# Kernel tuning notes

Measured on AMD Instinct MI355X. Metric: run time of the kernel, lower is better.

The kernel has to match this reference:

```python
import jax, jax.numpy as jnp
import numpy as np

M = 8192
K = 32

def setup_inputs() -> dict:
    key = jax.random.key(0)
    kw, ky = jax.random.split(key)
    W = jax.random.uniform(kw, (M, M), dtype=jnp.float32)  # nonnegative affinity
    Y = jax.random.normal(ky, (M, K), dtype=jnp.float32)
    return {"W": W, "Y": Y}

def reference(W, Y):
    # Random-walk Laplacian Rayleigh quotient: trace(Y^T (I - D^{-1} W) Y) / m,
    # with D = diag(row sums of W). Exploits diagonal D: D^{-1} W Y == (W @ Y) / d[:, None].
    m = Y.shape[0]
    d = jnp.sum(W, axis=1)                      # [m] row sums (diag of D)
    WY = W @ Y                                   # [m, k] thin matmul
    LY = Y - WY / d[:, None]                     # (I - D^{-1} W) Y without forming L
    loss = jnp.sum(Y * LY) / m                   # trace(Y^T L Y) / m
    return loss
```

## Files before the change

kernel.cpp:

```cpp
#include <hip/hip_runtime.h>

#define MDIM 8192
#define KD 32
#define SROW 260
#define TILES_PB 4
#define NBLOCKS 1024
#define NRED 32

typedef __attribute__((ext_vector_type(8))) short short8;
typedef __attribute__((ext_vector_type(4))) float f32x4;

__device__ __forceinline__ short f2bf(float f) {
    unsigned int u = __builtin_bit_cast(unsigned int, f);
    u = (u + 0x7FFFu + ((u >> 16) & 1u)) >> 16;
    return (short)(unsigned short)u;
}

__global__ __launch_bounds__(256)
void spectral_mfma(const float* __restrict__ W, const float* __restrict__ Y,
                   float* __restrict__ ws_s, float* __restrict__ ws_d) {
    __shared__ float YT[KD * SROW];

    const int tid  = threadIdx.x;
    const int wave = tid >> 6;
    const int lane = tid & 63;
    const int g    = lane >> 4;
    const int n    = lane & 15;

    const int rg = blockIdx.x >> 3;
    const int js = blockIdx.x & 7;
    const int rowBaseW = rg * 64 + wave * 16;
    const int rowW = rowBaseW + n;
    const float* Wrow = W + (size_t)rowW * MDIM;
    const int jbase0 = js * 1024;

    f32x4 acc1 = {0.f, 0.f, 0.f, 0.f};
    f32x4 acc2 = {0.f, 0.f, 0.f, 0.f};
    float dpart = 0.f;

    for (int tile = 0; tile < TILES_PB; ++tile) {
        const int jt = jbase0 + tile * 256;

        __syncthreads();

        float4 yr[8];
        {
            const float4* yp = (const float4*)(Y + (size_t)(jt + tid) * KD);
#pragma unroll
            for (int q = 0; q < 8; ++q) yr[q] = yp[q];
        }
        float4 wv[8][2];
#pragma unroll
        for (int jc = 0; jc < 8; ++jc) {
            const float* p = Wrow + jt + jc * 32 + g * 8;
            wv[jc][0] = *(const float4*)p;
            wv[jc][1] = *(const float4*)(p + 4);
        }
#pragma unroll
        for (int q = 0; q < 8; ++q) {
            YT[(4 * q + 0) * SROW + tid] = yr[q].x;
            YT[(4 * q + 1) * SROW + tid] = yr[q].y;
            YT[(4 * q + 2) * SROW + tid] = yr[q].z;
            YT[(4 * q + 3) * SROW + tid] = yr[q].w;
        }
        __syncthreads();

#pragma unroll
        for (int jc = 0; jc < 8; ++jc) {
            dpart += ((wv[jc][0].x + wv[jc][0].y) + (wv[jc][0].z + wv[jc][0].w))
                   + ((wv[jc][1].x + wv[jc][1].y) + (wv[jc][1].z + wv[jc][1].w));
            short8 a;
            a[0] = f2bf(wv[jc][0].x); a[1] = f2bf(wv[jc][0].y);
            a[2] = f2bf(wv[jc][0].z); a[3] = f2bf(wv[jc][0].w);
            a[4] = f2bf(wv[jc][1].x); a[5] = f2bf(wv[jc][1].y);
            a[6] = f2bf(wv[jc][1].z); a[7] = f2bf(wv[jc][1].w);

            const int jo = jc * 32 + g * 8;
            const float* b1p = &YT[n * SROW + jo];
            const float* b2p = &YT[(n + 16) * SROW + jo];
            float4 b1a = *(const float4*)b1p, b1b = *(const float4*)(b1p + 4);
            float4 b2a = *(const float4*)b2p, b2b = *(const float4*)(b2p + 4);
            short8 b1, b2;
            b1[0] = f2bf(b1a.x); b1[1] = f2bf(b1a.y); b1[2] = f2bf(b1a.z); b1[3] = f2bf(b1a.w);
            b1[4] = f2bf(b1b.x); b1[5] = f2bf(b1b.y); b1[6] = f2bf(b1b.z); b1[7] = f2bf(b1b.w);
            b2[0] = f2bf(b2a.x); b2[1] = f2bf(b2a.y); b2[2] = f2bf(b2a.z); b2[3] = f2bf(b2a.w);
            b2[4] = f2bf(b2b.x); b2[5] = f2bf(b2b.y); b2[6] = f2bf(b2b.z); b2[7] = f2bf(b2b.w);

            acc1 = __builtin_amdgcn_mfma_f32_16x16x32_bf16(a, b1, acc1, 0, 0, 0);
            acc2 = __builtin_amdgcn_mfma_f32_16x16x32_bf16(a, b2, acc2, 0, 0, 0);
        }
    }

#pragma unroll
    for (int r = 0; r < 4; ++r) {
        const int m = g * 4 + r;
        const int grow = rowBaseW + m;
        float ps = acc1[r] * Y[(size_t)grow * KD + n]
                 + acc2[r] * Y[(size_t)grow * KD + 16 + n];
        ps += __shfl_xor(ps, 1);
        ps += __shfl_xor(ps, 2);
        ps += __shfl_xor(ps, 4);
        ps += __shfl_xor(ps, 8);
        if (n == 0) atomicAdd(&ws_s[grow], ps);
    }
    float dv = dpart;
    dv += __shfl_xor(dv, 16);
    dv += __shfl_xor(dv, 32);
    if (g == 0) atomicAdd(&ws_d[rowBaseW + n], dv);
}

__global__ void zero_ws_kernel(float* __restrict__ ws_s, float* __restrict__ ws_d,
                               float* __restrict__ out) {
    const int i = blockIdx.x * 256 + threadIdx.x;
    ws_s[i] = 0.f;
    ws_d[i] = 0.f;
    if (i == 0) out[0] = 0.f;
}

__global__ void finalize_kernel(const float* __restrict__ Y,
                                const float* __restrict__ ws_s,
                                const float* __restrict__ ws_d,
                                float* __restrict__ out) {
    __shared__ float red[256];
    const int tid = threadIdx.x;
    const int i = blockIdx.x * 256 + tid;
    const float4* yp = (const float4*)(Y + (size_t)i * KD);
    float yy = 0.f;
#pragma unroll
    for (int q = 0; q < 8; ++q) {
        float4 y = yp[q];
        yy += y.x * y.x + y.y * y.y + y.z * y.z + y.w * y.w;
    }
    red[tid] = yy - ws_s[i] / ws_d[i];
    __syncthreads();
#pragma unroll
    for (int s = 128; s > 0; s >>= 1) {
        if (tid < s) red[tid] += red[tid + s];
        __syncthreads();
    }
    if (tid == 0) atomicAdd(out, red[0] * (1.0f / (float)MDIM));
}

extern "C" void kernel_launch(void* const* d_in, const int* in_sizes, int n_in,
                              void* d_out, int out_size, void* d_ws, size_t ws_size,
                              hipStream_t stream) {
    const float* W = (const float*)d_in[0];
    const float* Y = (const float*)d_in[1];
    float* out  = (float*)d_out;
    float* ws_s = (float*)d_ws;
    float* ws_d = ws_s + MDIM;

    zero_ws_kernel<<<NRED, 256, 0, stream>>>(ws_s, ws_d, out);
    spectral_mfma<<<NBLOCKS, 256, 0, stream>>>(W, Y, ws_s, ws_d);
    finalize_kernel<<<NRED, 256, 0, stream>>>(Y, ws_s, ws_d, out);
}
```

Measured before the change: 384.3 us.

## Pre-transpose Y to bf16 in global memory and compute row sums via MFMA

A prep kernel now converts Y into a transposed bf16 array in the workspace and zeroes the accumulators, replacing the separate zero kernel. The main kernel reads its B operands straight from global memory, so the shared-memory staging and both __syncthreads per tile go away. W is packed to bf16 with a truncating byte-permute instead of round-to-nearest-even, and the row sums d now come from a third MFMA against a ones vector instead of fp32 adds. The j range is split 16 ways for more blocks. In exchange, d is computed from bf16-truncated W, which costs accuracy, and B loads now hit global or cache memory instead of LDS.

```diff
diff --git a/kernel.cpp b/kernel.cpp
--- a/kernel.cpp
+++ b/kernel.cpp
@@ -2,119 +2,105 @@
 
 #define MDIM 8192
 #define KD 32
-#define SROW 260
-#define TILES_PB 4
-#define NBLOCKS 1024
+#define JSPLIT 16
+#define JWIN (MDIM / JSPLIT)
+#define NBLOCKS (128 * JSPLIT)
 #define NRED 32
 
 typedef __attribute__((ext_vector_type(8))) short short8;
 typedef __attribute__((ext_vector_type(4))) float f32x4;
 
-__device__ __forceinline__ short f2bf(float f) {
+union S8U { short8 s; uint4 u; };
+
+__device__ __forceinline__ unsigned short f2bf_rne(float f) {
     unsigned int u = __builtin_bit_cast(unsigned int, f);
     u = (u + 0x7FFFu + ((u >> 16) & 1u)) >> 16;
-    return (short)(unsigned short)u;
+    return (unsigned short)u;
+}
+
+__device__ __forceinline__ unsigned pk(float lo, float hi) {
+    return __builtin_amdgcn_perm(__builtin_bit_cast(unsigned, hi),
+                                 __builtin_bit_cast(unsigned, lo), 0x07060302u);
+}
+
+__global__ void prep_kernel(const float* __restrict__ Y, unsigned short* __restrict__ YT,
+                            float* __restrict__ ws_s, float* __restrict__ ws_d,
+                            float* __restrict__ out) {
+    const int j = blockIdx.x * 256 + threadIdx.x;
+    ws_s[j] = 0.f;
+    ws_d[j] = 0.f;
+    if (j == 0) out[0] = 0.f;
+    const float4* yp = (const float4*)(Y + (size_t)j * KD);
+#pragma unroll
+    for (int q = 0; q < 8; ++q) {
+        float4 v = yp[q];
+        YT[(size_t)(4 * q + 0) * MDIM + j] = f2bf_rne(v.x);
+        YT[(size_t)(4 * q + 1) * MDIM + j] = f2bf_rne(v.y);
+        YT[(size_t)(4 * q + 2) * MDIM + j] = f2bf_rne(v.z);
+        YT[(size_t)(4 * q + 3) * MDIM + j] = f2bf_rne(v.w);
+    }
 }
 
 __global__ __launch_bounds__(256)
-void spectral_mfma(const float* __restrict__ W, const float* __restrict__ Y,
+void spectral_mfma(const float* __restrict__ W, const unsigned short* __restrict__ YTb,
+                   const float* __restrict__ Y,
                    float* __restrict__ ws_s, float* __restrict__ ws_d) {
-    __shared__ float YT[KD * SROW];
-
     const int tid  = threadIdx.x;
     const int wave = tid >> 6;
     const int lane = tid & 63;
     const int g    = lane >> 4;
     const int n    = lane & 15;
 
-    const int rg = blockIdx.x >> 3;
-    const int js = blockIdx.x & 7;
-    const int rowBaseW = rg * 64 + wave * 16;
-    const int rowW = rowBaseW + n;
-    const float* Wrow = W + (size_t)rowW * MDIM;
-    const int jbase0 = js * 1024;
+    const int rg = blockIdx.x >> 4;
+    const int js = blockIdx.x & (JSPLIT - 1);
+    const int rowBase = rg * 64 + wave * 16;
+    const float* Wrow = W + (size_t)(rowBase + n) * MDIM;
+    const int j0 = js * JWIN;
 
     f32x4 acc1 = {0.f, 0.f, 0.f, 0.f};
     f32x4 acc2 = {0.f, 0.f, 0.f, 0.f};
-    float dpart = 0.f;
+    f32x4 acc3 = {0.f, 0.f, 0.f, 0.f};
 
-    for (int tile = 0; tile < TILES_PB; ++tile) {
-        const int jt = jbase0 + tile * 256;
+    S8U ones;
+    ones.u = make_uint4(0x3F803F80u, 0x3F803F80u, 0x3F803F80u, 0x3F803F80u);
 
-        __syncthreads();
+    const float* wp0 = Wrow + j0 + g * 8;
+    const unsigned short* bp0 = YTb + (size_t)n * MDIM + j0 + g * 8;
 
-        float4 yr[8];
-        {
-            const float4* yp = (const float4*)(Y + (size_t)(jt + tid) * KD);
-#pragma unroll
-            for (int q = 0; q < 8; ++q) yr[q] = yp[q];
-        }
-        float4 wv[8][2];
-#pragma unroll
-        for (int jc = 0; jc < 8; ++jc) {
-            const float* p = Wrow + jt + jc * 32 + g * 8;
-            wv[jc][0] = *(const float4*)p;
-            wv[jc][1] = *(const float4*)(p + 4);
-        }
-#pragma unroll
-        for (int q = 0; q < 8; ++q) {
-            YT[(4 * q + 0) * SROW + tid] = yr[q].x;
-            YT[(4 * q + 1) * SROW + tid] = yr[q].y;
-            YT[(4 * q + 2) * SROW + tid] = yr[q].z;
-            YT[(4 * q + 3) * SROW + tid] = yr[q].w;
-        }
-        __syncthreads();
+#pragma unroll 4
+    for (int it = 0; it < JWIN / 32; ++it) {
+        const float* wp = wp0 + it * 32;
+        float4 w0 = *(const float4*)wp;
+        float4 w1 = *(const float4*)(wp + 4);
+        const unsigned short* bp = bp0 + it * 32;
+        short8 b1 = *(const short8*)bp;
+        short8 b2 = *(const short8*)(bp + (size_t)16 * MDIM);
 
-#pragma unroll
-        for (int jc = 0; jc < 8; ++jc) {
-            dpart += ((wv[jc][0].x + wv[jc][0].y) + (wv[jc][0].z + wv[jc][0].w))
-                   + ((wv[jc][1].x + wv[jc][1].y) + (wv[jc][1].z + wv[jc][1].w));
-            short8 a;
-            a[0] = f2bf(wv[jc][0].x); a[1] = f2bf(wv[jc][0].y);
-            a[2] = f2bf(wv[jc][0].z); a[3] = f2bf(wv[jc][0].w);
-            a[4] = f2bf(wv[jc][1].x); a[5] = f2bf(wv[jc][1].y);
-            a[6] = f2bf(wv[jc][1].z); a[7] = f2bf(wv[jc][1].w);
+        S8U a;
+        a.u.x = pk(w0.x, w0.y);
+        a.u.y = pk(w0.z, w0.w);
+        a.u.z = pk(w1.x, w1.y);
+        a.u.w = pk(w1.z, w1.w);
 
-            const int jo = jc * 32 + g * 8;
-            const float* b1p = &YT[n * SROW + jo];
-            const float* b2p = &YT[(n + 16) * SROW + jo];
-            float4 b1a = *(const float4*)b1p, b1b = *(const float4*)(b1p + 4);
-            float4 b2a = *(const float4*)b2p, b2b = *(const float4*)(b2p + 4);
-            short8 b1, b2;
-            b1[0] = f2bf(b1a.x); b1[1] = f2bf(b1a.y); b1[2] = f2bf(b1a.z); b1[3] = f2bf(b1a.w);
-            b1[4] = f2bf(b1b.x); b1[5] = f2bf(b1b.y); b1[6] = f2bf(b1b.z); b1[7] = f2bf(b1b.w);
-            b2[0] = f2bf(b2a.x); b2[1] = f2bf(b2a.y); b2[2] = f2bf(b2a.z); b2[3] = f2bf(b2a.w);
-            b2[4] = f2bf(b2b.x); b2[5] = f2bf(b2b.y); b2[6] = f2bf(b2b.z); b2[7] = f2bf(b2b.w);
-
-            acc1 = __builtin_amdgcn_mfma_f32_16x16x32_bf16(a, b1, acc1, 0, 0, 0);
-            acc2 = __builtin_amdgcn_mfma_f32_16x16x32_bf16(a, b2, acc2, 0, 0, 0);
-        }
+        acc1 = __builtin_amdgcn_mfma_f32_16x16x32_bf16(a.s, b1, acc1, 0, 0, 0);
+        acc2 = __builtin_amdgcn_mfma_f32_16x16x32_bf16(a.s, b2, acc2, 0, 0, 0);
+        acc3 = __builtin_amdgcn_mfma_f32_16x16x32_bf16(a.s, ones.s, acc3, 0, 0, 0);
     }
 
 #pragma unroll
     for (int r = 0; r < 4; ++r) {
-        const int m = g * 4 + r;
-        const int grow = rowBaseW + m;
+        const int grow = rowBase + g * 4 + r;
         float ps = acc1[r] * Y[(size_t)grow * KD + n]
                  + acc2[r] * Y[(size_t)grow * KD + 16 + n];
         ps += __shfl_xor(ps, 1);
         ps += __shfl_xor(ps, 2);
         ps += __shfl_xor(ps, 4);
         ps += __shfl_xor(ps, 8);
-        if (n == 0) atomicAdd(&ws_s[grow], ps);
+        if (n == 0) {
+            atomicAdd(&ws_s[grow], ps);
+            atomicAdd(&ws_d[grow], acc3[r]);
+        }
     }
-    float dv = dpart;
-    dv += __shfl_xor(dv, 16);
-    dv += __shfl_xor(dv, 32);
-    if (g == 0) atomicAdd(&ws_d[rowBaseW + n], dv);
-}
-
-__global__ void zero_ws_kernel(float* __restrict__ ws_s, float* __restrict__ ws_d,
-                               float* __restrict__ out) {
-    const int i = blockIdx.x * 256 + threadIdx.x;
-    ws_s[i] = 0.f;
-    ws_d[i] = 0.f;
-    if (i == 0) out[0] = 0.f;
 }
 
 __global__ void finalize_kernel(const float* __restrict__ Y,
@@ -149,8 +135,9 @@
     float* out  = (float*)d_out;
     float* ws_s = (float*)d_ws;
     float* ws_d = ws_s + MDIM;
+    unsigned short* YTb = (unsigned short*)(ws_s + 2 * MDIM);
 
-    zero_ws_kernel<<<NRED, 256, 0, stream>>>(ws_s, ws_d, out);
-    spectral_mfma<<<NBLOCKS, 256, 0, stream>>>(W, Y, ws_s, ws_d);
+    prep_kernel<<<NRED, 256, 0, stream>>>(Y, YTb, ws_s, ws_d, out);
+    spectral_mfma<<<NBLOCKS, 256, 0, stream>>>(W, YTb, Y, ws_s, ws_d);
     finalize_kernel<<<NRED, 256, 0, stream>>>(Y, ws_s, ws_d, out);
 }
```

Result: faster. 361.6 us (-5.9%).
